# Optimization experiments

Measured on AMD Instinct MI355X. Metric: run time of the kernel, lower is better.

## Reference

```python
import jax, jax.numpy as jnp
import numpy as np

B, L, D, H = 2, 256, 512, 8
DH = D // H
EPS = 1e-12
NEG = -1000000000000000.0


def setup_inputs() -> dict:
    key = jax.random.key(0)
    ks = jax.random.split(key, 16)
    s = 0.02
    return {
        "inputs": jax.random.normal(ks[0], (B, L, D), jnp.float32),
        "pos_embedding": jax.random.normal(ks[1], (B, L, L, D), jnp.float32),
        "seq_mask": jnp.ones((B, L), jnp.int32),
        "Wq": jax.random.normal(ks[2], (D, D), jnp.float32) * s,
        "bq": jnp.zeros((D,), jnp.float32),
        "Wk": jax.random.normal(ks[3], (D, D), jnp.float32) * s,
        "bk": jnp.zeros((D,), jnp.float32),
        "Wv": jax.random.normal(ks[4], (D, D), jnp.float32) * s,
        "bv": jnp.zeros((D,), jnp.float32),
        "Wr": jax.random.normal(ks[5], (D, D), jnp.float32) * s,
        "br": jnp.zeros((D,), jnp.float32),
        "u": jax.random.normal(ks[6], (H, DH), jnp.float32),
        "v": jax.random.normal(ks[7], (H, DH), jnp.float32),
        "Wf": jax.random.normal(ks[8], (D, D), jnp.float32) * s,
        "bf": jnp.zeros((D,), jnp.float32),
        "gamma": jnp.ones((D,), jnp.float32),
        "beta": jnp.zeros((D,), jnp.float32),
    }


def _layer_norm(x, gamma, beta, eps):
    mu = jnp.mean(x, axis=-1, keepdims=True)
    var = jnp.mean(jnp.square(x - mu), axis=-1, keepdims=True)
    return (x - mu) * jax.lax.rsqrt(var + eps) * gamma + beta


def reference(inputs, pos_embedding, seq_mask, Wq, bq, Wk, bk, Wv, bv, Wr, br,
              u, v, Wf, bf, gamma, beta):
    b, l, d = inputs.shape
    # projections (nn.Linear: x @ W.T + b)
    q = (inputs @ Wq.T + bq).reshape(b, l, H, DH).transpose(0, 2, 1, 3)  # [B,H,L,DH]
    k = (inputs @ Wk.T + bk).reshape(b, l, H, DH).transpose(0, 2, 1, 3)
    vv = (inputs @ Wv.T + bv).reshape(b, l, H, DH).transpose(0, 2, 1, 3)
    rel = (pos_embedding @ Wr.T + br).reshape(b, l, l, H, DH)            # [B,L,L,H,DH]

    # A + C: content-content + content-bias
    A_C = jnp.einsum('bhid,bhjd->bhij', q + u[None, :, None, :], k)
    # B + D: position term against per-(i,j) relative embeddings
    B_D = jnp.einsum('bhid,bijhd->bhij', q + v[None, :, None, :], rel)

    score = (A_C + B_D) / np.sqrt(DH).astype(np.float32)
    invalid = (seq_mask == 0)[:, None, None, :]   # mask keys where seq_mask==0
    score = jnp.where(invalid, NEG, score)
    attn = jax.nn.softmax(score, axis=-1)

    ctx = jnp.einsum('bhij,bhjd->bhid', attn, vv)
    ctx = ctx.transpose(0, 2, 1, 3).reshape(b, l, d)

    # FFN (single dense) + residual + LayerNorm
    h = ctx @ Wf.T + bf
    return _layer_norm(h + inputs, gamma, beta, EPS)
```

## Files before the change

kernel.cpp:

```cpp
#include <hip/hip_runtime.h>
#include <cmath>


typedef __bf16 bf16x8 __attribute__((ext_vector_type(8)));
typedef float f32x4 __attribute__((ext_vector_type(4)));

__device__ __forceinline__ float4 ld4(const float* p) { return *reinterpret_cast<const float4*>(p); }
__device__ __forceinline__ void st4(float* p, float4 v) { *reinterpret_cast<float4*>(p) = v; }
__device__ __forceinline__ void fma4(float4& a, float s, const float4& v) {
    a.x = fmaf(s, v.x, a.x); a.y = fmaf(s, v.y, a.y);
    a.z = fmaf(s, v.z, a.z); a.w = fmaf(s, v.w, a.w);
}
__device__ __forceinline__ float dot4(const float4& a, const float4& b) {
    return a.x*b.x + a.y*b.y + a.z*b.z + a.w*b.w;
}
__device__ __forceinline__ unsigned short f2bf(float f) {
    unsigned int x = __float_as_uint(f);
    unsigned int r = x + 0x7FFFu + ((x >> 16) & 1u);
    return (unsigned short)(r >> 16);
}
__device__ __forceinline__ ushort4 cvt4u(float4 a) {
    ushort4 u;
    u.x = f2bf(a.x); u.y = f2bf(a.y); u.z = f2bf(a.z); u.w = f2bf(a.w);
    return u;
}
__device__ __forceinline__ bf16x8 cvt8(float4 a, float4 b) {
    bf16x8 r;
    r[0] = (__bf16)a.x; r[1] = (__bf16)a.y; r[2] = (__bf16)a.z; r[3] = (__bf16)a.w;
    r[4] = (__bf16)b.x; r[5] = (__bf16)b.y; r[6] = (__bf16)b.z; r[7] = (__bf16)b.w;
    return r;
}

__device__ __forceinline__ void mfma_tile(
        const float* __restrict__ Abase, int ldA,
        const float* __restrict__ Bbase, int ldB,
        int K, int lane, f32x4 acc[4]) {
    int koff = (lane >> 4) * 8;
    int rr = lane & 15;
    const float* ap = Abase + rr * ldA + koff;
    const float* bp = Bbase + rr * ldB + koff;
#pragma unroll 2
    for (int k0 = 0; k0 < K; k0 += 32) {
        float4 a0  = ld4(ap + k0),            a1  = ld4(ap + k0 + 4);
        float4 b00 = ld4(bp + k0),            b01 = ld4(bp + k0 + 4);
        float4 b10 = ld4(bp + 16*ldB + k0),   b11 = ld4(bp + 16*ldB + k0 + 4);
        float4 b20 = ld4(bp + 32*ldB + k0),   b21 = ld4(bp + 32*ldB + k0 + 4);
        float4 b30 = ld4(bp + 48*ldB + k0),   b31 = ld4(bp + 48*ldB + k0 + 4);
        bf16x8 af = cvt8(a0, a1);
        acc[0] = __builtin_amdgcn_mfma_f32_16x16x32_bf16(af, cvt8(b00, b01), acc[0], 0, 0, 0);
        acc[1] = __builtin_amdgcn_mfma_f32_16x16x32_bf16(af, cvt8(b10, b11), acc[1], 0, 0, 0);
        acc[2] = __builtin_amdgcn_mfma_f32_16x16x32_bf16(af, cvt8(b20, b21), acc[2], 0, 0, 0);
        acc[3] = __builtin_amdgcn_mfma_f32_16x16x32_bf16(af, cvt8(b30, b31), acc[3], 0, 0, 0);
    }
}

__global__ __launch_bounds__(256) void k_front(
        const float* __restrict__ x,
        const float* __restrict__ Wq, const float* __restrict__ Wk, const float* __restrict__ Wv,
        const float* __restrict__ bq, const float* __restrict__ bk, const float* __restrict__ bv,
        const float* __restrict__ Wr, const float* __restrict__ Wf,
        const float* __restrict__ u, const float* __restrict__ vbv, const float* __restrict__ br,
        float* __restrict__ qw, float* __restrict__ kw, float* __restrict__ vw,
        float* __restrict__ wrt, float* __restrict__ wft,
        float* __restrict__ c_ws, float* __restrict__ uk_ws, float* __restrict__ vwr_ws) {
    int id = blockIdx.x;
    int t = threadIdx.x;
    if (id < 192) {
        int mat = id >> 6, rem = id & 63;
        int m0 = (rem >> 3) * 64, n0 = (rem & 7) * 64;
        const float* W   = (mat == 0) ? Wq : (mat == 1) ? Wk : Wv;
        const float* bias= (mat == 0) ? bq : (mat == 1) ? bk : bv;
        float* out       = (mat == 0) ? qw : (mat == 1) ? kw : vw;
        int wv = t >> 6, lane = t & 63;
        f32x4 acc[4] = {{0,0,0,0},{0,0,0,0},{0,0,0,0},{0,0,0,0}};
        mfma_tile(x + (m0 + wv * 16) * 512, 512, W + n0 * 512, 512, 512, lane, acc);
        int h = n0 >> 6;
        int col = lane & 15, rbase = (lane >> 4) * 4;
        float rpart[4] = {0, 0, 0, 0};
#pragma unroll
        for (int c = 0; c < 4; c++) {
            int d = c * 16 + col;
            float bv_ = bias[n0 + d];
            float vbd = vbv[n0 + d];
            float brd = br[n0 + d];
            float ud  = u[n0 + d];
#pragma unroll
            for (int r = 0; r < 4; r++) {
                int m = m0 + wv * 16 + rbase + r;
                int b = m >> 8, i = m & 255;
                float val = acc[c][r] + bv_;
                out[((b * 8 + h) * 256 + i) * 64 + d] = val;
                if (mat == 0) rpart[r] += (val + vbd) * brd;
                else if (mat == 1) rpart[r] += val * ud;
            }
        }
        if (mat < 2) {
#pragma unroll
            for (int msk = 1; msk < 16; msk <<= 1) {
#pragma unroll
                for (int r = 0; r < 4; r++) rpart[r] += __shfl_xor(rpart[r], msk, 64);
            }
            if (col == 0) {
                float* dst = (mat == 0) ? c_ws : uk_ws;
#pragma unroll
                for (int r = 0; r < 4; r++) {
                    int m = m0 + wv * 16 + rbase + r;
                    int b = m >> 8, i = m & 255;
                    dst[(b * 8 + h) * 256 + i] = rpart[r];
                }
            }
        }
    } else {
        __shared__ float tile[64][65];
        __shared__ float vpart[4][64];
        int isWf = (id >= 256);
        int id2 = id - (isWf ? 256 : 192);
        const float* Wsrc = isWf ? Wf : Wr;
        float* Wdst = isWf ? wft : wrt;
        int n0 = (id2 >> 3) * 64, k0 = (id2 & 7) * 64;
        int h = n0 >> 6;
        int tx = t & 63, ty = t >> 6;
#pragma unroll
        for (int r = 0; r < 16; r++) {
            int row = ty * 16 + r;
            tile[row][tx] = Wsrc[(n0 + row) * 512 + k0 + tx];
        }
        __syncthreads();
#pragma unroll
        for (int r = 0; r < 16; r++) {
            int row = ty * 16 + r;
            Wdst[(k0 + row) * 512 + n0 + tx] = tile[tx][row];
        }
        if (!isWf) {
            float s = 0.f;
#pragma unroll
            for (int r = 0; r < 16; r++) s += vbv[n0 + ty * 16 + r] * tile[ty * 16 + r][tx];
            vpart[ty][tx] = s;
            __syncthreads();
            if (t < 64) vwr_ws[h * 512 + k0 + t] = vpart[0][t] + vpart[1][t] + vpart[2][t] + vpart[3][t];
        }
    }
}

__global__ __launch_bounds__(256) void k_mid(
        const float* __restrict__ qw, const float* __restrict__ kw,
        const float* __restrict__ wrt,
        const float* __restrict__ c_ws, const float* __restrict__ uk_ws,
        const float* __restrict__ vwr_ws,
        float* __restrict__ w_ws, float* __restrict__ ac_ws) {
    int id = blockIdx.x;
    int t = threadIdx.x, wv = t >> 6, lane = t & 63;
    int col = lane & 15, rbase = (lane >> 4) * 4;
    if (id < 512) {
        int h = id >> 6, rem = id & 63;
        int m0 = (rem >> 3) * 64, n0 = (rem & 7) * 64;
        int b = m0 >> 8, i0 = m0 & 255;
        f32x4 acc[4] = {{0,0,0,0},{0,0,0,0},{0,0,0,0},{0,0,0,0}};
        mfma_tile(qw + ((b * 8 + h) * 256 + i0 + wv * 16) * 64, 64,
                  wrt + (size_t)n0 * 512 + h * 64, 512, 64, lane, acc);
#pragma unroll
        for (int c = 0; c < 4; c++) {
            int n = n0 + c * 16 + col;
            float vw_ = vwr_ws[h * 512 + n];
#pragma unroll
            for (int r = 0; r < 4; r++) {
                int m = m0 + wv * 16 + rbase + r;
                w_ws[((size_t)m * 8 + h) * 512 + n] = acc[c][r] + vw_;
            }
        }
    } else {
        int id2 = id - 512;
        int bh = id2 >> 4, rem2 = id2 & 15;
        int b = bh >> 3, h = bh & 7;
        int i0 = (rem2 >> 2) * 64, j0 = (rem2 & 3) * 64;
        f32x4 acc[4] = {{0,0,0,0},{0,0,0,0},{0,0,0,0},{0,0,0,0}};
        mfma_tile(qw + ((b * 8 + h) * 256 + i0 + wv * 16) * 64, 64,
                  kw + ((b * 8 + h) * 256 + j0) * 64, 64, 64, lane, acc);
#pragma unroll
        for (int c = 0; c < 4; c++) {
            int j = j0 + c * 16 + col;
            float ukv = uk_ws[(b * 8 + h) * 256 + j];
#pragma unroll
            for (int r = 0; r < 4; r++) {
                int ii = i0 + wv * 16 + rbase + r;
                float ci = c_ws[(b * 8 + h) * 256 + ii];
                ac_ws[((size_t)(b * 256 + ii) * 8 + h) * 256 + j] = acc[c][r] + ukv + ci;
            }
        }
    }
}

__global__ __launch_bounds__(512, 4) void k_attn(
        const float* __restrict__ pos, const float* __restrict__ w_ws,
        const float* __restrict__ ac_ws, const float* __restrict__ vw,
        const int* __restrict__ seq_mask,
        const float* __restrict__ wft, const float* __restrict__ bf,
        const float* __restrict__ x,
        const float* __restrict__ gamma, const float* __restrict__ beta,
        float* __restrict__ outp) {
    int bi = blockIdx.x;
    int b = bi >> 8, i = bi & 255;
    int t = threadIdx.x;
    int wv = t >> 6, lane = t & 63;
    __shared__ unsigned short wl[16 * 512];
    __shared__ float sc[8][256];
    __shared__ unsigned short stage[8][2048];
    __shared__ float ctxl[512];
    __shared__ float lnred[8][2];

    {
        int h = t >> 6;
        int j = t & 63;
        const float* src = w_ws + ((size_t)bi * 8 + h) * 512 + j * 8;
        float4 a = ld4(src);
        float4 c = ld4(src + 4);
        char* dst = reinterpret_cast<char*>(wl) + (j >> 2) * 1024 + ((j & 3) * 16 + h) * 16;
        *reinterpret_cast<ushort4*>(dst)     = cvt4u(a);
        *reinterpret_cast<ushort4*>(dst + 8) = cvt4u(c);
    }
    __syncthreads();

    const float* pb = pos + (size_t)bi * (256 * 512);
    int jbase = wv * 32;
    char* sb = reinterpret_cast<char*>(&stage[wv][0]);
    int arow = lane & 15;
    int a_off = arow * 256 + (lane >> 4) * 16;
    int b_off = (lane & 15) * 16 + (lane >> 4) * 256;
    const char* wlc = reinterpret_cast<const char*>(wl);

#pragma unroll
    for (int jt = 0; jt < 2; jt++) {
        f32x4 acc = {0, 0, 0, 0};
#pragma unroll
        for (int eh = 0; eh < 4; eh++) {
            const float* src = pb + (size_t)(jbase + jt * 16 + (lane >> 5)) * 512
                             + eh * 128 + (lane & 31) * 4;
            float4 tmp[8];
#pragma unroll
            for (int s = 0; s < 8; s++) tmp[s] = ld4(src + (size_t)s * 2 * 512);
#pragma unroll
            for (int s = 0; s < 8; s++) {
                int row = (lane >> 5) + s * 2;
                *reinterpret_cast<ushort4*>(sb + row * 256 + (lane & 31) * 8) = cvt4u(tmp[s]);
            }
#pragma unroll
            for (int es = 0; es < 4; es++) {
                bf16x8 af = *reinterpret_cast<const bf16x8*>(sb + a_off + es * 64);
                int estep = eh * 4 + es;
                bf16x8 bf_ = *reinterpret_cast<const bf16x8*>(wlc + estep * 1024 + b_off);
                acc = __builtin_amdgcn_mfma_f32_16x16x32_bf16(af, bf_, acc, 0, 0, 0);
            }
        }
        int h = lane & 15;
        int rbase = (lane >> 4) * 4;
        if (h < 8) {
#pragma unroll
            for (int r = 0; r < 4; r++) sc[h][jbase + jt * 16 + rbase + r] = acc[r];
        }
    }
    __syncthreads();

    {
        int h = wv;
        const float* acrow = ac_ws + ((b * 256 + i) * 8 + h) * 256;
        float vals[4];
        float mx = -INFINITY;
#pragma unroll
        for (int r = 0; r < 4; r++) {
            int j = lane + r * 64;
            float s = (sc[h][j] + acrow[j]) * 0.125f;
            if (seq_mask[b * 256 + j] == 0) s = -1e15f;
            vals[r] = s;
            mx = fmaxf(mx, s);
        }
#pragma unroll
        for (int m = 32; m >= 1; m >>= 1) mx = fmaxf(mx, __shfl_xor(mx, m, 64));
        float sum = 0.f;
#pragma unroll
        for (int r = 0; r < 4; r++) { vals[r] = __expf(vals[r] - mx); sum += vals[r]; }
#pragma unroll
        for (int m = 32; m >= 1; m >>= 1) sum += __shfl_xor(sum, m, 64);
        float inv = 1.0f / sum;
#pragma unroll
        for (int r = 0; r < 4; r++) sc[h][lane + r * 64] = vals[r] * inv;
    }

    float4* part = reinterpret_cast<float4*>(&stage[0][0]);
    {
        int h = wv;
        int d4 = (lane & 15) * 4;
        int js = lane >> 4;
        const float* vbase = vw + (size_t)(b * 8 + h) * 256 * 64 + d4;
        float4 acc = {0, 0, 0, 0};
#pragma unroll 2
        for (int r = 0; r < 64; r += 4) {
            int j = js * 64 + r;
            float p0 = sc[h][j + 0], p1 = sc[h][j + 1];
            float p2 = sc[h][j + 2], p3 = sc[h][j + 3];
            float4 v0 = ld4(vbase + (size_t)(j + 0) * 64);
            float4 v1 = ld4(vbase + (size_t)(j + 1) * 64);
            float4 v2 = ld4(vbase + (size_t)(j + 2) * 64);
            float4 v3 = ld4(vbase + (size_t)(j + 3) * 64);
            fma4(acc, p0, v0); fma4(acc, p1, v1);
            fma4(acc, p2, v2); fma4(acc, p3, v3);
        }
        part[(h * 4 + js) * 16 + (lane & 15)] = acc;
    }
    {
        int h = wv;
        if ((lane >> 4) == 0) {
            int l = lane & 15;
            float4 a0 = part[(h * 4 + 0) * 16 + l], a1 = part[(h * 4 + 1) * 16 + l];
            float4 a2 = part[(h * 4 + 2) * 16 + l], a3 = part[(h * 4 + 3) * 16 + l];
            float4 o;
            o.x = a0.x + a1.x + a2.x + a3.x;
            o.y = a0.y + a1.y + a2.y + a3.y;
            o.z = a0.z + a1.z + a2.z + a3.z;
            o.w = a0.w + a1.w + a2.w + a3.w;
            st4(&ctxl[h * 64 + l * 4], o);
        }
    }
    __syncthreads();

    {
        int n = wv * 64 + lane;
        const float* wcol = wft + n;
        float acc = 0.f;
#pragma unroll 4
        for (int k0 = 0; k0 < 512; k0 += 8) {
            float4 c0 = ld4(&ctxl[k0]);
            float4 c1 = ld4(&ctxl[k0 + 4]);
            acc = fmaf(c0.x, wcol[(size_t)(k0 + 0) * 512], acc);
            acc = fmaf(c0.y, wcol[(size_t)(k0 + 1) * 512], acc);
            acc = fmaf(c0.z, wcol[(size_t)(k0 + 2) * 512], acc);
            acc = fmaf(c0.w, wcol[(size_t)(k0 + 3) * 512], acc);
            acc = fmaf(c1.x, wcol[(size_t)(k0 + 4) * 512], acc);
            acc = fmaf(c1.y, wcol[(size_t)(k0 + 5) * 512], acc);
            acc = fmaf(c1.z, wcol[(size_t)(k0 + 6) * 512], acc);
            acc = fmaf(c1.w, wcol[(size_t)(k0 + 7) * 512], acc);
        }
        float v = acc + bf[n] + x[(size_t)(b * 256 + i) * 512 + n];
        float s = v, q = v * v;
#pragma unroll
        for (int m = 32; m >= 1; m >>= 1) {
            s += __shfl_xor(s, m, 64);
            q += __shfl_xor(q, m, 64);
        }
        if (lane == 0) { lnred[wv][0] = s; lnred[wv][1] = q; }
        __syncthreads();
        float ts = 0.f, tq = 0.f;
#pragma unroll
        for (int w2 = 0; w2 < 8; w2++) { ts += lnred[w2][0]; tq += lnred[w2][1]; }
        float mu = ts * (1.0f / 512.0f);
        float var = tq * (1.0f / 512.0f) - mu * mu;
        float rstd = rsqrtf(var + 1e-12f);
        outp[(size_t)(b * 256 + i) * 512 + n] = (v - mu) * rstd * gamma[n] + beta[n];
    }
}

extern "C" void kernel_launch(void* const* d_in, const int* in_sizes, int n_in,
                              void* d_out, int out_size, void* d_ws, size_t ws_size,
                              hipStream_t stream) {
    const float* x     = (const float*)d_in[0];
    const float* pos   = (const float*)d_in[1];
    const int*   smask = (const int*)d_in[2];
    const float* Wq = (const float*)d_in[3];
    const float* bq = (const float*)d_in[4];
    const float* Wk = (const float*)d_in[5];
    const float* bk = (const float*)d_in[6];
    const float* Wv = (const float*)d_in[7];
    const float* bv = (const float*)d_in[8];
    const float* Wr = (const float*)d_in[9];
    const float* br = (const float*)d_in[10];
    const float* u  = (const float*)d_in[11];
    const float* vb = (const float*)d_in[12];
    const float* Wf = (const float*)d_in[13];
    const float* bf = (const float*)d_in[14];
    const float* gamma = (const float*)d_in[15];
    const float* beta  = (const float*)d_in[16];
    float* out = (float*)d_out;

    float* ws = (float*)d_ws;
    float* q_ws   = ws;
    float* k_ws   = q_ws  + 262144;
    float* v_ws   = k_ws  + 262144;
    float* w_ws   = v_ws  + 262144;
    float* ac_ws  = w_ws  + 2097152;
    float* wrt_ws = ac_ws + 1048576;
    float* wft_ws = wrt_ws + 262144;
    float* c_ws   = wft_ws + 262144;
    float* uk_ws  = c_ws  + 4096;
    float* vwr_ws = uk_ws + 4096;

    k_front<<<dim3(320), 256, 0, stream>>>(x, Wq, Wk, Wv, bq, bk, bv, Wr, Wf, u, vb, br,
                                           q_ws, k_ws, v_ws, wrt_ws, wft_ws,
                                           c_ws, uk_ws, vwr_ws);
    k_mid<<<dim3(768), 256, 0, stream>>>(q_ws, k_ws, wrt_ws, c_ws, uk_ws, vwr_ws, w_ws, ac_ws);
    k_attn<<<dim3(512), 512, 0, stream>>>(pos, w_ws, ac_ws, v_ws, smask,
                                          wft_ws, bf, x, gamma, beta, out);
}
```

Before: 103.4 us.

## Fuse mid-stage projections into attention kernel and drop intermediate workspaces

Removes the k_mid launch and computes, inside each attention block, the q·Wr projection row (w), the q+u dot k content scores, and the q+v dot br bias term directly in registers and shared memory. This avoids writing and re-reading the large w_ws and ac_ws buffers and saves one kernel launch. In exchange each block now does scalar fp32 dot products over Wr columns and K rows instead of the MFMA tiles, which adds compute and global reads to every attention block.

```diff
diff --git a/kernel.cpp b/kernel.cpp
--- a/kernel.cpp
+++ b/kernel.cpp
@@ -59,10 +59,8 @@
         const float* __restrict__ Wq, const float* __restrict__ Wk, const float* __restrict__ Wv,
         const float* __restrict__ bq, const float* __restrict__ bk, const float* __restrict__ bv,
         const float* __restrict__ Wr, const float* __restrict__ Wf,
-        const float* __restrict__ u, const float* __restrict__ vbv, const float* __restrict__ br,
         float* __restrict__ qw, float* __restrict__ kw, float* __restrict__ vw,
-        float* __restrict__ wrt, float* __restrict__ wft,
-        float* __restrict__ c_ws, float* __restrict__ uk_ws, float* __restrict__ vwr_ws) {
+        float* __restrict__ wrt, float* __restrict__ wft) {
     int id = blockIdx.x;
     int t = threadIdx.x;
     if (id < 192) {
@@ -76,49 +74,24 @@
         mfma_tile(x + (m0 + wv * 16) * 512, 512, W + n0 * 512, 512, 512, lane, acc);
         int h = n0 >> 6;
         int col = lane & 15, rbase = (lane >> 4) * 4;
-        float rpart[4] = {0, 0, 0, 0};
 #pragma unroll
         for (int c = 0; c < 4; c++) {
             int d = c * 16 + col;
             float bv_ = bias[n0 + d];
-            float vbd = vbv[n0 + d];
-            float brd = br[n0 + d];
-            float ud  = u[n0 + d];
 #pragma unroll
             for (int r = 0; r < 4; r++) {
                 int m = m0 + wv * 16 + rbase + r;
                 int b = m >> 8, i = m & 255;
-                float val = acc[c][r] + bv_;
-                out[((b * 8 + h) * 256 + i) * 64 + d] = val;
-                if (mat == 0) rpart[r] += (val + vbd) * brd;
-                else if (mat == 1) rpart[r] += val * ud;
-            }
-        }
-        if (mat < 2) {
-#pragma unroll
-            for (int msk = 1; msk < 16; msk <<= 1) {
-#pragma unroll
-                for (int r = 0; r < 4; r++) rpart[r] += __shfl_xor(rpart[r], msk, 64);
-            }
-            if (col == 0) {
-                float* dst = (mat == 0) ? c_ws : uk_ws;
-#pragma unroll
-                for (int r = 0; r < 4; r++) {
-                    int m = m0 + wv * 16 + rbase + r;
-                    int b = m >> 8, i = m & 255;
-                    dst[(b * 8 + h) * 256 + i] = rpart[r];
-                }
+                out[((b * 8 + h) * 256 + i) * 64 + d] = acc[c][r] + bv_;
             }
         }
     } else {
         __shared__ float tile[64][65];
-        __shared__ float vpart[4][64];
         int isWf = (id >= 256);
         int id2 = id - (isWf ? 256 : 192);
         const float* Wsrc = isWf ? Wf : Wr;
         float* Wdst = isWf ? wft : wrt;
         int n0 = (id2 >> 3) * 64, k0 = (id2 & 7) * 64;
-        int h = n0 >> 6;
         int tx = t & 63, ty = t >> 6;
 #pragma unroll
         for (int r = 0; r < 16; r++) {
@@ -131,68 +104,14 @@
             int row = ty * 16 + r;
             Wdst[(k0 + row) * 512 + n0 + tx] = tile[tx][row];
         }
-        if (!isWf) {
-            float s = 0.f;
-#pragma unroll
-            for (int r = 0; r < 16; r++) s += vbv[n0 + ty * 16 + r] * tile[ty * 16 + r][tx];
-            vpart[ty][tx] = s;
-            __syncthreads();
-            if (t < 64) vwr_ws[h * 512 + k0 + t] = vpart[0][t] + vpart[1][t] + vpart[2][t] + vpart[3][t];
-        }
-    }
-}
-
-__global__ __launch_bounds__(256) void k_mid(
-        const float* __restrict__ qw, const float* __restrict__ kw,
+    }
+}
+
+__global__ __launch_bounds__(512, 4) void k_attn(
+        const float* __restrict__ pos,
+        const float* __restrict__ qw, const float* __restrict__ kw, const float* __restrict__ vw,
         const float* __restrict__ wrt,
-        const float* __restrict__ c_ws, const float* __restrict__ uk_ws,
-        const float* __restrict__ vwr_ws,
-        float* __restrict__ w_ws, float* __restrict__ ac_ws) {
-    int id = blockIdx.x;
-    int t = threadIdx.x, wv = t >> 6, lane = t & 63;
-    int col = lane & 15, rbase = (lane >> 4) * 4;
-    if (id < 512) {
-        int h = id >> 6, rem = id & 63;
-        int m0 = (rem >> 3) * 64, n0 = (rem & 7) * 64;
-        int b = m0 >> 8, i0 = m0 & 255;
-        f32x4 acc[4] = {{0,0,0,0},{0,0,0,0},{0,0,0,0},{0,0,0,0}};
-        mfma_tile(qw + ((b * 8 + h) * 256 + i0 + wv * 16) * 64, 64,
-                  wrt + (size_t)n0 * 512 + h * 64, 512, 64, lane, acc);
-#pragma unroll
-        for (int c = 0; c < 4; c++) {
-            int n = n0 + c * 16 + col;
-            float vw_ = vwr_ws[h * 512 + n];
-#pragma unroll
-            for (int r = 0; r < 4; r++) {
-                int m = m0 + wv * 16 + rbase + r;
-                w_ws[((size_t)m * 8 + h) * 512 + n] = acc[c][r] + vw_;
-            }
-        }
-    } else {
-        int id2 = id - 512;
-        int bh = id2 >> 4, rem2 = id2 & 15;
-        int b = bh >> 3, h = bh & 7;
-        int i0 = (rem2 >> 2) * 64, j0 = (rem2 & 3) * 64;
-        f32x4 acc[4] = {{0,0,0,0},{0,0,0,0},{0,0,0,0},{0,0,0,0}};
-        mfma_tile(qw + ((b * 8 + h) * 256 + i0 + wv * 16) * 64, 64,
-                  kw + ((b * 8 + h) * 256 + j0) * 64, 64, 64, lane, acc);
-#pragma unroll
-        for (int c = 0; c < 4; c++) {
-            int j = j0 + c * 16 + col;
-            float ukv = uk_ws[(b * 8 + h) * 256 + j];
-#pragma unroll
-            for (int r = 0; r < 4; r++) {
-                int ii = i0 + wv * 16 + rbase + r;
-                float ci = c_ws[(b * 8 + h) * 256 + ii];
-                ac_ws[((size_t)(b * 256 + ii) * 8 + h) * 256 + j] = acc[c][r] + ukv + ci;
-            }
-        }
-    }
-}
-
-__global__ __launch_bounds__(512, 4) void k_attn(
-        const float* __restrict__ pos, const float* __restrict__ w_ws,
-        const float* __restrict__ ac_ws, const float* __restrict__ vw,
+        const float* __restrict__ uv, const float* __restrict__ vbv, const float* __restrict__ br,
         const int* __restrict__ seq_mask,
         const float* __restrict__ wft, const float* __restrict__ bf,
         const float* __restrict__ x,
@@ -207,16 +126,46 @@
     __shared__ unsigned short stage[8][2048];
     __shared__ float ctxl[512];
     __shared__ float lnred[8][2];
-
-    {
-        int h = t >> 6;
-        int j = t & 63;
-        const float* src = w_ws + ((size_t)bi * 8 + h) * 512 + j * 8;
-        float4 a = ld4(src);
-        float4 c = ld4(src + 4);
-        char* dst = reinterpret_cast<char*>(wl) + (j >> 2) * 1024 + ((j & 3) * 16 + h) * 16;
+    __shared__ float qvb[8][64];
+    __shared__ float qu[8][64];
+    __shared__ float c_l[8];
+
+    {
+        int h = t >> 6, d = t & 63;
+        float qv = qw[((size_t)(b * 8 + h) * 256 + i) * 64 + d];
+        qvb[h][d] = qv + vbv[h * 64 + d];
+        qu[h][d]  = qv + uv[h * 64 + d];
+    }
+    float ac_reg[4];
+    {
+        int h = wv;
+        int e0 = lane * 8;
+        float wacc[8];
+#pragma unroll
+        for (int j = 0; j < 8; j++) {
+            const float* wr = wrt + (size_t)(e0 + j) * 512 + h * 64;
+            float s = 0.f;
+#pragma unroll
+            for (int d4 = 0; d4 < 64; d4 += 4) s += dot4(ld4(wr + d4), ld4(&qvb[h][d4]));
+            wacc[j] = s;
+        }
+        float4 a = {wacc[0], wacc[1], wacc[2], wacc[3]};
+        float4 c = {wacc[4], wacc[5], wacc[6], wacc[7]};
+        char* dst = reinterpret_cast<char*>(wl) + (lane >> 2) * 1024 + ((lane & 3) * 16 + h) * 16;
         *reinterpret_cast<ushort4*>(dst)     = cvt4u(a);
         *reinterpret_cast<ushort4*>(dst + 8) = cvt4u(c);
+        float cs = qvb[h][lane] * br[h * 64 + lane];
+#pragma unroll
+        for (int m = 32; m >= 1; m >>= 1) cs += __shfl_xor(cs, m, 64);
+        if (lane == 0) c_l[h] = cs;
+#pragma unroll
+        for (int r = 0; r < 4; r++) {
+            const float* kp = kw + ((size_t)(b * 8 + h) * 256 + lane + r * 64) * 64;
+            float s = 0.f;
+#pragma unroll
+            for (int d4 = 0; d4 < 64; d4 += 4) s += dot4(ld4(kp + d4), ld4(&qu[h][d4]));
+            ac_reg[r] = s;
+        }
     }
     __syncthreads();
 
@@ -262,13 +211,13 @@
 
     {
         int h = wv;
-        const float* acrow = ac_ws + ((b * 256 + i) * 8 + h) * 256;
+        float ch = c_l[h];
         float vals[4];
         float mx = -INFINITY;
 #pragma unroll
         for (int r = 0; r < 4; r++) {
             int j = lane + r * 64;
-            float s = (sc[h][j] + acrow[j]) * 0.125f;
+            float s = (sc[h][j] + ac_reg[r] + ch) * 0.125f;
             if (seq_mask[b * 256 + j] == 0) s = -1e15f;
             vals[r] = s;
             mx = fmaxf(mx, s);
@@ -384,18 +333,12 @@
     float* q_ws   = ws;
     float* k_ws   = q_ws  + 262144;
     float* v_ws   = k_ws  + 262144;
-    float* w_ws   = v_ws  + 262144;
-    float* ac_ws  = w_ws  + 2097152;
-    float* wrt_ws = ac_ws + 1048576;
+    float* wrt_ws = v_ws  + 262144;
     float* wft_ws = wrt_ws + 262144;
-    float* c_ws   = wft_ws + 262144;
-    float* uk_ws  = c_ws  + 4096;
-    float* vwr_ws = uk_ws + 4096;
-
-    k_front<<<dim3(320), 256, 0, stream>>>(x, Wq, Wk, Wv, bq, bk, bv, Wr, Wf, u, vb, br,
-                                           q_ws, k_ws, v_ws, wrt_ws, wft_ws,
-                                           c_ws, uk_ws, vwr_ws);
-    k_mid<<<dim3(768), 256, 0, stream>>>(q_ws, k_ws, wrt_ws, c_ws, uk_ws, vwr_ws, w_ws, ac_ws);
-    k_attn<<<dim3(512), 512, 0, stream>>>(pos, w_ws, ac_ws, v_ws, smask,
+
+    k_front<<<dim3(320), 256, 0, stream>>>(x, Wq, Wk, Wv, bq, bk, bv, Wr, Wf,
+                                           q_ws, k_ws, v_ws, wrt_ws, wft_ws);
+    k_attn<<<dim3(512), 512, 0, stream>>>(pos, q_ws, k_ws, v_ws, wrt_ws,
+                                          u, vb, br, smask,
                                           wft_ws, bf, x, gamma, beta, out);
 }
```

Measured after the change: 401.3 us. 3.88x slower.
